# Kernel tuning notes

Hardware: AMD Instinct MI355X
Metric: run time of the kernel (lower is better)

Reference implementation:

```python
import jax, jax.numpy as jnp
import numpy as np

LN_EPS = 1e-5


def _layernorm(h, g, b):
    m = jnp.mean(h, axis=-1, keepdims=True)
    v = jnp.mean(jnp.square(h - m), axis=-1, keepdims=True)
    return g * (h - m) / jnp.sqrt(v + LN_EPS) + b


def _film_dense(x, cond, W, b, ln_g, ln_b, gW, gb, bW, bb):
    # Dense -> LayerNorm -> FiLM affine from cond -> relu
    h = _layernorm(x @ W + b, ln_g, ln_b)
    gamma = cond @ gW + gb
    beta = cond @ bW + bb
    return jax.nn.relu((1.0 + gamma) * h + beta)


def _forward(x, y, embW1, embb1, embW2, embb2,
             tW, tb, t_ln_g, t_ln_b, t_gW, t_gb, t_bW, t_bb, toW, tob,
             sW, sb, s_ln_g, s_ln_b, s_gW, s_gb, s_bW, s_bb, soW, sob):
    L = embW1.shape[0]
    masks = jnp.asarray(
        [[1, 1, 0, 0] if i % 2 == 0 else [0, 0, 1, 1] for i in range(L)],
        dtype=x.dtype)  # [L, 4]
    z = x
    log_det_inv = jnp.zeros(x.shape[0], dtype=x.dtype)
    for i in range(L):  # small fixed structural loop over coupling layers
        mask = masks[i]
        rmask = 1.0 - mask
        z_masked = z * mask
        # per-layer label embedding MLP (relu, relu)
        y_emb = jax.nn.relu(jax.nn.relu(y @ embW1[i] + embb1[i]) @ embW2[i] + embb2[i])
        t_h = _film_dense(z_masked, y_emb, tW[i], tb[i], t_ln_g[i], t_ln_b[i],
                          t_gW[i], t_gb[i], t_bW[i], t_bb[i])
        t_final = t_h @ toW[i] + tob[i]
        s_h = _film_dense(z_masked, y_emb, sW[i], sb[i], s_ln_g[i], s_ln_b[i],
                          s_gW[i], s_gb[i], s_bW[i], s_bb[i])
        s_final = jnp.tanh(s_h @ soW[i] + sob[i])
        transformed = (z * rmask) * jnp.exp(s_final) + t_final
        z = z * mask + transformed * rmask
        log_det_inv = log_det_inv + jnp.sum(s_final * rmask, axis=-1)
    return z, log_det_inv


def setup_inputs() -> dict:
    key = jax.random.key(0)
    ks = jax.random.split(key, 16)
    B, L, D, H, C = 262144, 8, 4, 32, 4
    s = 0.1  # small weight scale keeps exp(s) well-behaved
    return {
        "x": jax.random.normal(ks[0], (B, D), jnp.float32),
        "y": jax.random.uniform(ks[1], (B, C), jnp.float32),
        "embW1": jax.random.normal(ks[2], (L, C, H), jnp.float32) * s,
        "embb1": jnp.zeros((L, H), jnp.float32),
        "embW2": jax.random.normal(ks[3], (L, H, H), jnp.float32) * s,
        "embb2": jnp.zeros((L, H), jnp.float32),
        "tW": jax.random.normal(ks[4], (L, D, H), jnp.float32) * s,
        "tb": jnp.zeros((L, H), jnp.float32),
        "t_ln_g": jnp.ones((L, H), jnp.float32),
        "t_ln_b": jnp.zeros((L, H), jnp.float32),
        "t_gW": jax.random.normal(ks[5], (L, H, H), jnp.float32) * s,
        "t_gb": jnp.zeros((L, H), jnp.float32),
        "t_bW": jax.random.normal(ks[6], (L, H, H), jnp.float32) * s,
        "t_bb": jnp.zeros((L, H), jnp.float32),
        "toW": jax.random.normal(ks[7], (L, H, D), jnp.float32) * s,
        "tob": jnp.zeros((L, D), jnp.float32),
        "sW": jax.random.normal(ks[8], (L, D, H), jnp.float32) * s,
        "sb": jnp.zeros((L, H), jnp.float32),
        "s_ln_g": jnp.ones((L, H), jnp.float32),
        "s_ln_b": jnp.zeros((L, H), jnp.float32),
        "s_gW": jax.random.normal(ks[9], (L, H, H), jnp.float32) * s,
        "s_gb": jnp.zeros((L, H), jnp.float32),
        "s_bW": jax.random.normal(ks[10], (L, H, H), jnp.float32) * s,
        "s_bb": jnp.zeros((L, H), jnp.float32),
        "soW": jax.random.normal(ks[11], (L, H, D), jnp.float32) * s,
        "sob": jnp.zeros((L, D), jnp.float32),
    }


def reference(x, y, embW1, embb1, embW2, embb2,
              tW, tb, t_ln_g, t_ln_b, t_gW, t_gb, t_bW, t_bb, toW, tob,
              sW, sb, s_ln_g, s_ln_b, s_gW, s_gb, s_bW, s_bb, soW, sob):
    return _forward(x, y, embW1, embb1, embW2, embb2,
                    tW, tb, t_ln_g, t_ln_b, t_gW, t_gb, t_bW, t_bb, toW, tob,
                    sW, sb, s_ln_g, s_ln_b, s_gW, s_gb, s_bW, s_bb, soW, sob)
```

## Files before the change

### kernel.cpp

```cpp
#include <hip/hip_runtime.h>
#include <math.h>

#define LN_EPS 1e-5f
#define LOG2E 1.44269504088896f
#define LN2   0.69314718055994531f

typedef float f4 __attribute__((ext_vector_type(4)));
typedef float f2 __attribute__((ext_vector_type(2)));
typedef int   i4 __attribute__((ext_vector_type(4)));
typedef short bf16x8 __attribute__((ext_vector_type(8)));

#define WS_PARM_OFF 98304
#define WS_UNIF_OFF 139264
#define WS_NEED 140032

#define WAITLGKM() do { \
    asm volatile("s_waitcnt lgkmcnt(0)" ::: "memory"); \
    __builtin_amdgcn_sched_barrier(0); \
} while (0)

__device__ __forceinline__ unsigned short rne_bf16(float f) {
    unsigned u = __builtin_bit_cast(unsigned, f);
    unsigned r = (u + 0x7FFFu + ((u >> 16) & 1u)) >> 16;
    return (unsigned short)r;
}

__device__ __forceinline__ unsigned cvt_pk_bf16(float lo, float hi) {
    unsigned r;
    asm("v_cvt_pk_bf16_f32 %0, %1, %2" : "=v"(r) : "v"(lo), "v"(hi));
    return r;
}

template <int CTRL>
__device__ __forceinline__ float dpp_add_step(float v) {
    int t = __builtin_amdgcn_update_dpp(0, __builtin_bit_cast(int, v), CTRL, 0xf, 0xf, true);
    return v + __builtin_bit_cast(float, t);
}
__device__ __forceinline__ float reduce16(float v) {
    v = dpp_add_step<0xB1>(v);
    v = dpp_add_step<0x4E>(v);
    v = dpp_add_step<0x141>(v);
    v = dpp_add_step<0x140>(v);
    return v;
}

__global__ void preproc_kernel(
    const float* __restrict__ embW2, const float* __restrict__ embb2,
    const float* __restrict__ tW, const float* __restrict__ tb,
    const float* __restrict__ t_ln_g, const float* __restrict__ t_ln_b,
    const float* __restrict__ t_gW, const float* __restrict__ t_gb,
    const float* __restrict__ t_bW, const float* __restrict__ t_bb,
    const float* __restrict__ toW, const float* __restrict__ tob,
    const float* __restrict__ sW, const float* __restrict__ sb,
    const float* __restrict__ s_ln_g, const float* __restrict__ s_ln_b,
    const float* __restrict__ s_gW, const float* __restrict__ s_gb,
    const float* __restrict__ s_bW, const float* __restrict__ s_bb,
    const float* __restrict__ soW, const float* __restrict__ sob,
    unsigned short* __restrict__ ws16, float* __restrict__ wsP,
    float* __restrict__ wsU)
{
    const int i = blockIdx.x;
    const int tid = threadIdx.x;
    const int parity = i & 1;
    const int ka = parity ? 2 : 0, pa = parity ? 0 : 2;

    const float* fsrc[6] = {embW2 + i * 1024, embW2 + i * 1024,
                            t_gW + i * 1024, t_bW + i * 1024,
                            s_gW + i * 1024, s_bW + i * 1024};
    for (int e = tid; e < 6144; e += 256) {
        int s = e >> 10, e10 = e & 1023;
        int half = e10 >> 9, ln = (e10 >> 3) & 63, j = e10 & 7;
        int p8 = (ln >> 4) * 8 + j;
        int k = (s >= 2) ? ((p8 >> 1) | ((p8 & 1) << 4)) : p8;
        int c = half * 16 + (ln & 15);
        float w = fsrc[s][k * 32 + c];
        unsigned short hv = rne_bf16(w);
        if (s == 1) {
            float whi = __builtin_bit_cast(float, (unsigned)hv << 16);
            hv = rne_bf16(w - whi);
        }
        ws16[i * 6144 + s * 1024 + e10] = hv;
    }

    if (tid < 32) {
        int p = tid >> 4, r = tid & 15;
        const float* W   = (p ? sW : tW) + i * 128;
        const float* b   = (p ? sb : tb) + i * 32;
        const float* lng = (p ? s_ln_g : t_ln_g) + i * 32;
        const float* lnb = (p ? s_ln_b : t_ln_b) + i * 32;
        const float* gb  = (p ? s_gb : t_gb) + i * 32;
        const float* bb  = (p ? s_bb : t_bb) + i * 32;
        const float* ow  = (p ? soW : toW) + i * 128;
        float sc = p ? (2.0f * LOG2E) : 1.0f;
        int cL = r, cH = r + 16;
        float* dst = wsP + i * 640 + p * 320;
        f4 v0 = {W[ka*32+cL]*lng[cL], W[(ka+1)*32+cL]*lng[cL], b[cL]*lng[cL], lng[cL]};
        f4 v1 = {W[ka*32+cH]*lng[cH], W[(ka+1)*32+cH]*lng[cH], b[cH]*lng[cH], lng[cH]};
        f4 v2 = {lnb[cL], lnb[cH], gb[cL], gb[cH]};
        f4 v3 = {bb[cL], bb[cH], ow[cL*4+pa]*sc, ow[cL*4+pa+1]*sc};
        f4 v4 = {ow[cH*4+pa]*sc, ow[cH*4+pa+1]*sc, embb2[i*32+cL], embb2[i*32+cH]};
        *(f4*)(dst + 0*64 + r*4) = v0;
        *(f4*)(dst + 1*64 + r*4) = v1;
        *(f4*)(dst + 2*64 + r*4) = v2;
        *(f4*)(dst + 3*64 + r*4) = v3;
        *(f4*)(dst + 4*64 + r*4) = v4;
    } else if (tid < 34) {
        int p = tid - 32;
        const float* W  = (p ? sW : tW) + i * 128;
        const float* b  = (p ? sb : tb) + i * 32;
        const float* ob = (p ? sob : tob) + i * 4;
        float sc = p ? (2.0f * LOG2E) : 1.0f;
        float S0=0,S1=0,Sb=0,Q00=0,Q11=0,Qbb=0,Q01=0,Q0b=0,Q1b=0;
        for (int c = 0; c < 32; ++c) {
            float w0 = W[ka*32+c], w1 = W[(ka+1)*32+c], bc = b[c];
            S0+=w0; S1+=w1; Sb+=bc;
            Q00+=w0*w0; Q11+=w1*w1; Qbb+=bc*bc;
            Q01+=w0*w1; Q0b+=w0*bc; Q1b+=w1*bc;
        }
        const float inv32 = 1.0f / 32.0f;
        float* u = wsU + (i*2+p)*12;
        u[0]=S0*inv32; u[1]=S1*inv32; u[2]=Sb*inv32;
        u[3]=Q00*inv32; u[4]=2.0f*Q01*inv32; u[5]=2.0f*Q0b*inv32;
        u[6]=Q11*inv32; u[7]=2.0f*Q1b*inv32; u[8]=Qbb*inv32;
        u[9]=ob[pa]*sc*(1.0f/16.0f); u[10]=ob[pa+1]*sc*(1.0f/16.0f);
        u[11]=0.0f;
    }
}

__device__ __forceinline__ void film_path(
    const unsigned short* __restrict__ fb, int slotg, int slotb, int lane,
    int kaf, int path, const float* Z, const float* ST,
    const bf16x8 a2[2], const f4 pv[5], const float* __restrict__ u,
    float (&f0)[2][4], float (&f1)[2][4])
{
    const int g = lane >> 4;
    bf16x8 gh0 = *(const bf16x8*)(fb + slotg * 1024 + lane * 8);
    bf16x8 gh1 = *(const bf16x8*)(fb + slotg * 1024 + 512 + lane * 8);
    bf16x8 bh0 = *(const bf16x8*)(fb + slotb * 1024 + lane * 8);
    bf16x8 bh1 = *(const bf16x8*)(fb + slotb * 1024 + 512 + lane * 8);
    float gbL = pv[2][2], gbH = pv[2][3], bbL = pv[3][0], bbH = pv[3][1];
    f4 cg0 = {gbL, gbL, gbL, gbL}, cg1 = {gbH, gbH, gbH, gbH};
    f4 cb0 = {bbL, bbL, bbL, bbL}, cb1 = {bbH, bbH, bbH, bbH};
    f4 gacc[2][2], bacc[2][2];
    #pragma unroll
    for (int t = 0; t < 2; ++t) {
        gacc[t][0] = __builtin_amdgcn_mfma_f32_16x16x32_bf16(a2[t], gh0, cg0, 0, 0, 0);
        gacc[t][1] = __builtin_amdgcn_mfma_f32_16x16x32_bf16(a2[t], gh1, cg1, 0, 0, 0);
        bacc[t][0] = __builtin_amdgcn_mfma_f32_16x16x32_bf16(a2[t], bh0, cb0, 0, 0, 0);
        bacc[t][1] = __builtin_amdgcn_mfma_f32_16x16x32_bf16(a2[t], bh1, cb1, 0, 0, 0);
    }
    float ob0 = u[9], ob1 = u[10];
    float wk0L=pv[0][0], wk1L=pv[0][1], bL=pv[0][2], lngL=pv[0][3];
    float wk0H=pv[1][0], wk1H=pv[1][1], bH=pv[1][2], lngH=pv[1][3];
    float lnbL=pv[2][0], lnbH=pv[2][1];
    float owL0=pv[3][2], owL1=pv[3][3], owH0=pv[4][0], owH1=pv[4][1];
    #pragma unroll
    for (int t = 0; t < 2; ++t) {
        #pragma unroll
        for (int q = 0; q < 4; ++q) {
            int rowl = 16 * t + 4 * g + q;
            f2 zkv = *(const f2*)(Z + rowl * 4 + kaf);
            f2 st  = *(const f2*)(ST + rowl * 4 + path * 2);
            float hL = fmaf(zkv[0], wk0L, fmaf(zkv[1], wk1L, bL));
            float hH = fmaf(zkv[0], wk0H, fmaf(zkv[1], wk1H, bH));
            float nL = fmaf(hL, st[1], fmaf(st[0], lngL, lnbL));
            float nH = fmaf(hH, st[1], fmaf(st[0], lngH, lnbH));
            float gL = gacc[t][0][q], gH = gacc[t][1][q];
            float btL = bacc[t][0][q], btH = bacc[t][1][q];
            float thL = fmaxf(fmaf(gL, nL, nL + btL), 0.0f);
            float thH = fmaxf(fmaf(gH, nH, nH + btH), 0.0f);
            float p0 = fmaf(thL, owL0, fmaf(thH, owH0, ob0));
            float p1 = fmaf(thL, owL1, fmaf(thH, owH1, ob1));
            f0[t][q] = reduce16(p0);
            f1[t][q] = reduce16(p1);
        }
    }
}

__global__ __launch_bounds__(256, 1) void realnvp_mfma(
    const float* __restrict__ x, const float* __restrict__ y,
    const float* __restrict__ embW1, const float* __restrict__ embb1,
    const unsigned short* __restrict__ ws16,
    const float* __restrict__ wsP, const float* __restrict__ wsU,
    float* __restrict__ out_z, float* __restrict__ out_ld)
{
    __shared__ __align__(16) unsigned char ldsbuf[4 * 4096];
    const int lane = threadIdx.x & 63;
    const int wv = threadIdx.x >> 6;
    const int r = lane & 15, g = lane >> 4;
    const int rs = lane & 31, hw = lane >> 5;
    unsigned char* T = ldsbuf + wv * 4096;
    float* Z  = (float*)(ldsbuf + wv * 4096 + 2560);
    float* ST = (float*)(ldsbuf + wv * 4096 + 3072);
    float* FB = (float*)(ldsbuf + wv * 4096 + 3584);
    const int row0 = (blockIdx.x * 4 + wv) * 32;

    if (lane < 32) {
        *(f4*)(Z + rs * 4) = *(const f4*)(x + (size_t)(row0 + rs) * 4);
    }
    f4 y4[2];
    y4[0] = *(const f4*)(y + (size_t)(row0 + r) * 4);
    y4[1] = *(const f4*)(y + (size_t)(row0 + 16 + r) * 4);
    float ld2 = 0.0f;
    WAITLGKM();

    #pragma unroll 1
    for (int i = 0; i < 8; ++i) {
        const int parity = i & 1;
        const int kaf = parity ? 2 : 0;
        const int pa  = parity ? 0 : 2;
        const unsigned short* fb = ws16 + i * 6144;
        const float* pP = wsP + i * 640;
        const float* uT = wsU + (i * 2) * 12;
        const float* uS = uT + 12;

        {
            f2 zk = *(const f2*)(Z + rs * 4 + kaf);
            const float* ub = wsU + (i * 2 + hw) * 12;
            f4 u0 = *(const f4*)(ub);
            f4 u1 = *(const f4*)(ub + 4);
            f4 u2 = *(const f4*)(ub + 8);
            float za = zk[0], zb = zk[1];
            float m   = fmaf(za, u0[0], fmaf(zb, u0[1], u0[2]));
            float ex2 = fmaf(za, fmaf(za, u0[3], fmaf(zb, u1[0], u1[1])),
                             fmaf(zb, fmaf(zb, u1[2], u1[3]), u2[0]));
            float var = fmaxf(fmaf(-m, m, ex2), 0.0f);
            float rstd = __builtin_amdgcn_rsqf(var + LN_EPS);
            f2 stv = {-m * rstd, rstd};
            *(f2*)(ST + rs * 4 + hw * 2) = stv;
        }

        f4 ptv[5];
        #pragma unroll
        for (int v = 0; v < 5; ++v) ptv[v] = *(const f4*)(pP + v * 64 + r * 4);

        const float* W1 = embW1 + i * 128;
        f4 w1a[4], w1b[4];
        #pragma unroll
        for (int c = 0; c < 4; ++c) {
            w1a[c] = *(const f4*)(W1 + c * 32 + g * 8);
            w1b[c] = *(const f4*)(W1 + c * 32 + g * 8 + 4);
        }
        f4 b1a = *(const f4*)(embb1 + i * 32 + g * 8);
        f4 b1b = *(const f4*)(embb1 + i * 32 + g * 8 + 4);
        bf16x8 a1[2];
        #pragma unroll
        for (int t = 0; t < 2; ++t) {
            unsigned aw[4];
            #pragma unroll
            for (int jp = 0; jp < 4; ++jp) {
                const int j0 = 2 * jp, j1 = 2 * jp + 1;
                float aL = (j0 < 4) ? b1a[j0 & 3] : b1b[j0 & 3];
                float aH = (j1 < 4) ? b1a[j1 & 3] : b1b[j1 & 3];
                #pragma unroll
                for (int c = 0; c < 4; ++c) {
                    aL = fmaf(y4[t][c], (j0 < 4) ? w1a[c][j0 & 3] : w1b[c][j0 & 3], aL);
                    aH = fmaf(y4[t][c], (j1 < 4) ? w1a[c][j1 & 3] : w1b[c][j1 & 3], aH);
                }
                aw[jp] = cvt_pk_bf16(fmaxf(aL, 0.0f), fmaxf(aH, 0.0f));
            }
            i4 ai = {(int)aw[0], (int)aw[1], (int)aw[2], (int)aw[3]};
            a1[t] = __builtin_bit_cast(bf16x8, ai);
        }

        bf16x8 w2h0 = *(const bf16x8*)(fb + lane * 8);
        bf16x8 w2h1 = *(const bf16x8*)(fb + 512 + lane * 8);
        bf16x8 w2l0 = *(const bf16x8*)(fb + 1024 + lane * 8);
        bf16x8 w2l1 = *(const bf16x8*)(fb + 1536 + lane * 8);
        float b2L = ptv[4][2], b2H = ptv[4][3];
        f4 c2L = {b2L, b2L, b2L, b2L}, c2H = {b2H, b2H, b2H, b2H};
        f4 e2a[2][2];
        #pragma unroll
        for (int t = 0; t < 2; ++t) {
            e2a[t][0] = __builtin_amdgcn_mfma_f32_16x16x32_bf16(a1[t], w2h0, c2L, 0, 0, 0);
            e2a[t][0] = __builtin_amdgcn_mfma_f32_16x16x32_bf16(a1[t], w2l0, e2a[t][0], 0, 0, 0);
            e2a[t][1] = __builtin_amdgcn_mfma_f32_16x16x32_bf16(a1[t], w2h1, c2H, 0, 0, 0);
            e2a[t][1] = __builtin_amdgcn_mfma_f32_16x16x32_bf16(a1[t], w2l1, e2a[t][1], 0, 0, 0);
        }

        #pragma unroll
        for (int t = 0; t < 2; ++t)
            #pragma unroll
            for (int q = 0; q < 4; ++q) {
                int rowl = 16 * t + 4 * g + q;
                float vl = fmaxf(e2a[t][0][q], 0.0f);
                float vh = fmaxf(e2a[t][1][q], 0.0f);
                *(unsigned*)(T + rowl * 80 + r * 4) = cvt_pk_bf16(vl, vh);
            }
        WAITLGKM();
        bf16x8 a2[2];
        a2[0] = *(const bf16x8*)(T + r * 80 + g * 16);
        a2[1] = *(const bf16x8*)(T + (16 + r) * 80 + g * 16);

        float tf0[2][4], tf1[2][4], sf0[2][4], sf1[2][4];
        film_path(fb, 2, 3, lane, kaf, 0, Z, ST, a2, ptv, uT, tf0, tf1);
        f4 psv[5];
        #pragma unroll
        for (int v = 0; v < 5; ++v) psv[v] = *(const f4*)(pP + 320 + v * 64 + r * 4);
        film_path(fb, 4, 5, lane, kaf, 1, Z, ST, a2, psv, uS, sf0, sf1);

        if (r == 0) {
            #pragma unroll
            for (int t = 0; t < 2; ++t)
                #pragma unroll
                for (int q = 0; q < 4; ++q) {
                    int rowl = 16 * t + 4 * g + q;
                    f4 v = {tf0[t][q], sf0[t][q], tf1[t][q], sf1[t][q]};
                    *(f4*)(FB + rowl * 4) = v;
                }
        }
        WAITLGKM();

        {
            int d = pa + hw;
            f2 fv = *(const f2*)(FB + rs * 4 + hw * 2);
            float e  = __builtin_amdgcn_exp2f(fv[1]);
            float rc = __builtin_amdgcn_rcpf(e + 1.0f);
            float s2 = fmaf(-2.0f * LOG2E, rc, LOG2E);
            float eA = __builtin_amdgcn_exp2f(s2);
            float zo = Z[rs * 4 + d];
            Z[rs * 4 + d] = fmaf(zo, eA, fv[0]);
            ld2 += s2;
        }
        WAITLGKM();
    }

    float oth = __shfl(ld2, lane ^ 32, 64);
    float ldv = (ld2 + oth) * LN2;
    if (lane < 32) {
        f4 zo = *(const f4*)(Z + rs * 4);
        *(f4*)(out_z + (size_t)(row0 + rs) * 4) = zo;
        out_ld[row0 + rs] = ldv;
    }
}

extern "C" void kernel_launch(void* const* d_in, const int* in_sizes, int n_in,
                              void* d_out, int out_size, void* d_ws, size_t ws_size,
                              hipStream_t stream) {
    const float* x      = (const float*)d_in[0];
    const float* y      = (const float*)d_in[1];
    const float* embW1  = (const float*)d_in[2];
    const float* embb1  = (const float*)d_in[3];
    const float* embW2  = (const float*)d_in[4];
    const float* embb2  = (const float*)d_in[5];
    const float* tW     = (const float*)d_in[6];
    const float* tb     = (const float*)d_in[7];
    const float* t_ln_g = (const float*)d_in[8];
    const float* t_ln_b = (const float*)d_in[9];
    const float* t_gW   = (const float*)d_in[10];
    const float* t_gb   = (const float*)d_in[11];
    const float* t_bW   = (const float*)d_in[12];
    const float* t_bb   = (const float*)d_in[13];
    const float* toW    = (const float*)d_in[14];
    const float* tob    = (const float*)d_in[15];
    const float* sW     = (const float*)d_in[16];
    const float* sb     = (const float*)d_in[17];
    const float* s_ln_g = (const float*)d_in[18];
    const float* s_ln_b = (const float*)d_in[19];
    const float* s_gW   = (const float*)d_in[20];
    const float* s_gb   = (const float*)d_in[21];
    const float* s_bW   = (const float*)d_in[22];
    const float* s_bb   = (const float*)d_in[23];
    const float* soW    = (const float*)d_in[24];
    const float* sob    = (const float*)d_in[25];

    if (ws_size < WS_NEED) return;
    unsigned short* ws16 = (unsigned short*)d_ws;
    float* wsP = (float*)((char*)d_ws + WS_PARM_OFF);
    float* wsU = (float*)((char*)d_ws + WS_UNIF_OFF);

    int B = in_sizes[0] / 4;
    float* out_z  = (float*)d_out;
    float* out_ld = out_z + (size_t)B * 4;

    hipLaunchKernelGGL(preproc_kernel, dim3(8), dim3(256), 0, stream,
                       embW2, embb2, tW, tb, t_ln_g, t_ln_b, t_gW, t_gb,
                       t_bW, t_bb, toW, tob, sW, sb, s_ln_g, s_ln_b,
                       s_gW, s_gb, s_bW, s_bb, soW, sob, ws16, wsP, wsU);
    hipLaunchKernelGGL(realnvp_mfma, dim3(B / 128), dim3(256), 0, stream,
                       x, y, embW1, embb1, ws16, wsP, wsU, out_z, out_ld);
}
```

Before: 119.3 us.

## Pad per-row LDS stride to six floats and raise launch-bounds occupancy hint

Changes the per-row stride of the Z, ST and FB LDS scratch arrays from 4 to 6 floats, splitting vec4 accesses into two vec2 accesses, to reduce LDS bank conflicts on the strided row reads inside film_path. It also enlarges the per-wave LDS region and raises the launch_bounds min-blocks hint from 1 to 6, which asks the compiler to cap register use for higher occupancy. The register cap risks spills, and the vec2 splits add extra LDS instructions.

```diff
diff --git a/kernel.cpp b/kernel.cpp
--- a/kernel.cpp
+++ b/kernel.cpp
@@ -13,6 +13,12 @@
 #define WS_PARM_OFF 98304
 #define WS_UNIF_OFF 139264
 #define WS_NEED 140032
+
+#define WV_STRIDE 4864
+#define Z_OFF  2560
+#define ST_OFF 3328
+#define FB_OFF 4096
+#define RSTRIDE 6
 
 #define WAITLGKM() do { \
     asm volatile("s_waitcnt lgkmcnt(0)" ::: "memory"); \
@@ -159,8 +165,8 @@
         #pragma unroll
         for (int q = 0; q < 4; ++q) {
             int rowl = 16 * t + 4 * g + q;
-            f2 zkv = *(const f2*)(Z + rowl * 4 + kaf);
-            f2 st  = *(const f2*)(ST + rowl * 4 + path * 2);
+            f2 zkv = *(const f2*)(Z + rowl * RSTRIDE + kaf);
+            f2 st  = *(const f2*)(ST + rowl * RSTRIDE + path * 2);
             float hL = fmaf(zkv[0], wk0L, fmaf(zkv[1], wk1L, bL));
             float hH = fmaf(zkv[0], wk0H, fmaf(zkv[1], wk1H, bH));
             float nL = fmaf(hL, st[1], fmaf(st[0], lngL, lnbL));
@@ -177,26 +183,29 @@
     }
 }
 
-__global__ __launch_bounds__(256, 1) void realnvp_mfma(
+__global__ __launch_bounds__(256, 6) void realnvp_mfma(
     const float* __restrict__ x, const float* __restrict__ y,
     const float* __restrict__ embW1, const float* __restrict__ embb1,
     const unsigned short* __restrict__ ws16,
     const float* __restrict__ wsP, const float* __restrict__ wsU,
     float* __restrict__ out_z, float* __restrict__ out_ld)
 {
-    __shared__ __align__(16) unsigned char ldsbuf[4 * 4096];
+    __shared__ __align__(16) unsigned char ldsbuf[4 * WV_STRIDE];
     const int lane = threadIdx.x & 63;
     const int wv = threadIdx.x >> 6;
     const int r = lane & 15, g = lane >> 4;
     const int rs = lane & 31, hw = lane >> 5;
-    unsigned char* T = ldsbuf + wv * 4096;
-    float* Z  = (float*)(ldsbuf + wv * 4096 + 2560);
-    float* ST = (float*)(ldsbuf + wv * 4096 + 3072);
-    float* FB = (float*)(ldsbuf + wv * 4096 + 3584);
+    unsigned char* T = ldsbuf + wv * WV_STRIDE;
+    float* Z  = (float*)(ldsbuf + wv * WV_STRIDE + Z_OFF);
+    float* ST = (float*)(ldsbuf + wv * WV_STRIDE + ST_OFF);
+    float* FB = (float*)(ldsbuf + wv * WV_STRIDE + FB_OFF);
     const int row0 = (blockIdx.x * 4 + wv) * 32;
 
     if (lane < 32) {
-        *(f4*)(Z + rs * 4) = *(const f4*)(x + (size_t)(row0 + rs) * 4);
+        f4 xv = *(const f4*)(x + (size_t)(row0 + rs) * 4);
+        f2 lo = {xv.x, xv.y}, hi = {xv.z, xv.w};
+        *(f2*)(Z + rs * RSTRIDE) = lo;
+        *(f2*)(Z + rs * RSTRIDE + 2) = hi;
     }
     f4 y4[2];
     y4[0] = *(const f4*)(y + (size_t)(row0 + r) * 4);
@@ -215,7 +224,7 @@
         const float* uS = uT + 12;
 
         {
-            f2 zk = *(const f2*)(Z + rs * 4 + kaf);
+            f2 zk = *(const f2*)(Z + rs * RSTRIDE + kaf);
             const float* ub = wsU + (i * 2 + hw) * 12;
             f4 u0 = *(const f4*)(ub);
             f4 u1 = *(const f4*)(ub + 4);
@@ -227,7 +236,7 @@
             float var = fmaxf(fmaf(-m, m, ex2), 0.0f);
             float rstd = __builtin_amdgcn_rsqf(var + LN_EPS);
             f2 stv = {-m * rstd, rstd};
-            *(f2*)(ST + rs * 4 + hw * 2) = stv;
+            *(f2*)(ST + rs * RSTRIDE + hw * 2) = stv;
         }
 
         f4 ptv[5];
@@ -305,21 +314,23 @@
                 #pragma unroll
                 for (int q = 0; q < 4; ++q) {
                     int rowl = 16 * t + 4 * g + q;
-                    f4 v = {tf0[t][q], sf0[t][q], tf1[t][q], sf1[t][q]};
-                    *(f4*)(FB + rowl * 4) = v;
+                    f2 lo = {tf0[t][q], sf0[t][q]};
+                    f2 hi = {tf1[t][q], sf1[t][q]};
+                    *(f2*)(FB + rowl * RSTRIDE) = lo;
+                    *(f2*)(FB + rowl * RSTRIDE + 2) = hi;
                 }
         }
         WAITLGKM();
 
         {
             int d = pa + hw;
-            f2 fv = *(const f2*)(FB + rs * 4 + hw * 2);
+            f2 fv = *(const f2*)(FB + rs * RSTRIDE + hw * 2);
             float e  = __builtin_amdgcn_exp2f(fv[1]);
             float rc = __builtin_amdgcn_rcpf(e + 1.0f);
             float s2 = fmaf(-2.0f * LOG2E, rc, LOG2E);
             float eA = __builtin_amdgcn_exp2f(s2);
-            float zo = Z[rs * 4 + d];
-            Z[rs * 4 + d] = fmaf(zo, eA, fv[0]);
+            float zo = Z[rs * RSTRIDE + d];
+            Z[rs * RSTRIDE + d] = fmaf(zo, eA, fv[0]);
             ld2 += s2;
         }
         WAITLGKM();
@@ -328,7 +339,9 @@
     float oth = __shfl(ld2, lane ^ 32, 64);
     float ldv = (ld2 + oth) * LN2;
     if (lane < 32) {
-        f4 zo = *(const f4*)(Z + rs * 4);
+        f2 lo = *(const f2*)(Z + rs * RSTRIDE);
+        f2 hi = *(const f2*)(Z + rs * RSTRIDE + 2);
+        f4 zo = {lo[0], lo[1], hi[0], hi[1]};
         *(f4*)(out_z + (size_t)(row0 + rs) * 4) = zo;
         out_ld[row0 + rs] = ldv;
     }
```

After: 340.7 us. 2.86x slower.
